# Performance work log

Hardware: AMD Instinct MI355X
Metric: run time of the kernel (lower is better)

The kernel has to match this reference:

```python
import jax, jax.numpy as jnp
import numpy as np

H, W, D = 60, 60, 36            # voxel grid dims (x, y, z)
GRID = 0.08                      # voxel size in meters
SCALE_MULT = 3.0                 # radius multiplier
CHUNK = 7200                     # point-chunk size; 129600 / 7200 = 18 chunks
P = 2048                         # number of Gaussians
C = 13                           # semantic channels


def setup_inputs() -> dict:
    key = jax.random.key(0)
    k1, k2, k3, k4, k5 = jax.random.split(key, 5)
    # query points = voxel centers, guaranteed in-range for the int-bin asserts
    ii, jj, kk = jnp.meshgrid(jnp.arange(H), jnp.arange(W), jnp.arange(D), indexing='ij')
    pts = (jnp.stack([ii, jj, kk], axis=-1).reshape(-1, 3).astype(jnp.float32) + 0.5) * GRID
    pts = pts[None]  # [1, N, 3]
    lo = jnp.array([0.1, 0.1, 0.1], jnp.float32)
    hi = jnp.array([H, W, D], jnp.float32) * GRID - 0.1
    means3D = jax.random.uniform(k1, (1, P, 3), dtype=jnp.float32) * (hi - lo) + lo
    scales = jax.random.uniform(k2, (1, P, 3), minval=0.03, maxval=0.2, dtype=jnp.float32)
    # random rotations via QR -> SPD covariance Sigma = Q diag(s^2) Q^T
    A = jax.random.normal(k3, (P, 3, 3), dtype=jnp.float32)
    Q, _ = jnp.linalg.qr(A)
    cov3D = jnp.einsum('pij,pj,pkj->pik', Q, scales[0] ** 2, Q)[None]  # [1,P,3,3]
    opacities = jax.random.uniform(k4, (1, P), minval=0.1, maxval=1.0, dtype=jnp.float32)
    semantics = jax.random.normal(k5, (1, P, C), dtype=jnp.float32)
    origin_use = jnp.zeros((3,), jnp.float32)
    return {"pts": pts, "means3D": means3D, "opacities": opacities,
            "semantics": semantics, "scales": scales, "cov3D": cov3D,
            "origin_use": origin_use}


def _sym_inv6(packed):
    # packed: [P,6] = (xx, yy, zz, xy, yz, xz) of a symmetric 3x3 covariance
    a, b, c, d, e, f = (packed[:, i] for i in range(6))
    det = a * (b * c - e * e) - d * (d * c - e * f) + f * (d * e - b * f)
    ixx = (b * c - e * e) / det
    iyy = (a * c - f * f) / det
    izz = (a * b - d * d) / det
    ixy = (e * f - d * c) / det
    iyz = (d * f - a * e) / det
    ixz = (d * e - b * f) / det
    return ixx, iyy, izz, ixy, iyz, ixz


def _forward(pts, means3D, opacities, semantics, scales, cov3D, origin_use):
    pts = pts[0]                    # [N,3], no grad in original
    means3D = means3D[0]            # [P,3]
    opacities = opacities[0]        # [P]
    semantics = semantics[0]        # [P,C]
    scales = jax.lax.stop_gradient(scales[0])   # detached in original
    cov3D = cov3D[0]                # [P,3,3]

    radii = jnp.ceil(scales.max(-1) * SCALE_MULT / GRID).astype(jnp.int32)  # [P]
    m_int = ((jax.lax.stop_gradient(means3D) - origin_use) / GRID).astype(jnp.int32)  # [P,3]
    packed = cov3D.reshape(-1, 9)[:, jnp.array([0, 4, 8, 1, 5, 2])]  # [P,6]
    ixx, iyy, izz, ixy, iyz, ixz = _sym_inv6(packed)  # per-Gaussian inverse cov entries

    N = pts.shape[0]
    pts_c = pts.reshape(N // CHUNK, CHUNK, 3)

    def chunk_fn(p):  # p: [CHUNK,3]
        p_int = ((p - origin_use) / GRID).astype(jnp.int32)
        dx = p[:, 0:1] - means3D[None, :, 0]   # [CHUNK,P]
        dy = p[:, 1:2] - means3D[None, :, 1]
        dz = p[:, 2:3] - means3D[None, :, 2]
        quad = (ixx * dx * dx + iyy * dy * dy + izz * dz * dz
                + 2.0 * (ixy * dx * dy + iyz * dy * dz + ixz * dx * dz))
        inbox = (jnp.abs(p_int[:, None, :] - m_int[None, :, :])
                 <= radii[None, :, None]).all(-1)          # [CHUNK,P] box/bin test
        w = jnp.where(inbox, opacities[None, :] * jnp.exp(-0.5 * quad), 0.0)
        return w @ semantics                                # [CHUNK,C]

    logits = jax.lax.map(chunk_fn, pts_c).reshape(N, C)
    return logits


def reference(pts, means3D, opacities, semantics, scales, cov3D, origin_use):
    return _forward(pts, means3D, opacities, semantics, scales, cov3D, origin_use)
```

## Files before the change

### kernel.cpp

```cpp
#include <hip/hip_runtime.h>


constexpr int   HH      = 60;
constexpr int   WW      = 60;
constexpr int   DD      = 36;
constexpr int   P_N     = 2048;
constexpr int   C_N     = 13;
constexpr int   BXD     = 15;
constexpr int   BYD     = 15;
constexpr int   BZD     = 9;
constexpr int   NBRICK  = BXD * BYD * BZD;
constexpr int   CAP     = 192;
constexpr float GRID_SZ = 0.08f;

__global__ __launch_bounds__(256) void agg_fused(const float* __restrict__ means,
                                                 const float* __restrict__ opac,
                                                 const float* __restrict__ sem,
                                                 const float* __restrict__ scales,
                                                 const float* __restrict__ cov,
                                                 const float* __restrict__ origin,
                                                 float* __restrict__ out) {
    __shared__ int    s_idx[CAP];
    __shared__ int    s_cnt;
    __shared__ float4 s_mem[CAP * 6];
    float (*s_acc)[64][C_N] = (float (*)[64][C_N])s_mem;

    const int b = (int)blockIdx.x;
    const int bk = b % BZD; const int rem = b / BZD;
    const int bj = rem % BYD; const int bi = rem / BYD;
    const int i0 = bi * 4, j0 = bj * 4, k0 = bk * 4;

    const float ox = origin[0], oy = origin[1], oz = origin[2];

    if (threadIdx.x == 0) s_cnt = 0;
    __syncthreads();

    for (int g = (int)threadIdx.x; g < P_N; g += 256) {
        const float mx = means[g * 3 + 0], my = means[g * 3 + 1], mz = means[g * 3 + 2];
        const float sx = scales[g * 3 + 0], sy = scales[g * 3 + 1], sz = scales[g * 3 + 2];
        const float smax = fmaxf(sx, fmaxf(sy, sz));
        const int rad = (int)ceilf(smax * 3.0f / GRID_SZ);
        const int mix = (int)((mx - ox) / GRID_SZ);
        const int miy = (int)((my - oy) / GRID_SZ);
        const int miz = (int)((mz - oz) / GRID_SZ);
        const bool ov = (mix - rad <= i0 + 3) && (mix + rad >= i0)
                     && (miy - rad <= j0 + 3) && (miy + rad >= j0)
                     && (miz - rad <= k0 + 3) && (miz + rad >= k0);
        if (ov) {
            int xlo = max(mix - rad - i0, 0), xhi = min(mix + rad - i0, 3);
            int ylo = max(miy - rad - j0, 0), yhi = min(miy + rad - j0, 3);
            int zlo = max(miz - rad - k0, 0), zhi = min(miz + rad - k0, 3);
            unsigned mx4 = (0xFu >> (3 - xhi)) & (0xFu << xlo);
            unsigned my4 = (0xFu >> (3 - yhi)) & (0xFu << ylo);
            unsigned mz4 = (0xFu >> (3 - zhi)) & (0xFu << zlo);
            unsigned ent = (unsigned)g | (mx4 << 12) | (my4 << 16) | (mz4 << 20);
            int t = atomicAdd(&s_cnt, 1);
            if (t < CAP) s_idx[t] = (int)ent;
        }
    }
    __syncthreads();
    const int cnt = min(s_cnt, CAP);

    for (int e = (int)threadIdx.x; e < cnt; e += 256) {
        const int ent = s_idx[e];
        const int g = ent & 0xFFF;
        const float* cv = cov + g * 9;
        const float a = cv[0], bb = cv[4], c = cv[8], d = cv[1], e5 = cv[5], f = cv[2];
        const float det = a * (bb * c - e5 * e5) - d * (d * c - e5 * f)
                        + f * (d * e5 - bb * f);
        const float kD = -0.5f * 1.44269504088896340736f;
        const float kO = -1.44269504088896340736f;
        float4 r0, r1, r2, r3, r4, r5;
        r0.x = means[g * 3 + 0]; r0.y = means[g * 3 + 1]; r0.z = means[g * 3 + 2];
        r0.w = __log2f(opac[g]);
        r1.x = kD * (bb * c - e5 * e5) / det;
        r1.y = kD * (a * c - f * f) / det;
        r1.z = kD * (a * bb - d * d) / det;
        r1.w = kO * (e5 * f - d * c) / det;
        r2.x = kO * (d * f - a * e5) / det;
        r2.y = kO * (d * e5 - bb * f) / det;
        const float* sm = sem + g * C_N;
        r2.z = sm[0];  r2.w = sm[1];
        r3.x = sm[2];  r3.y = sm[3];  r3.z = sm[4];  r3.w = sm[5];
        r4.x = sm[6];  r4.y = sm[7];  r4.z = sm[8];  r4.w = sm[9];
        r5.x = sm[10]; r5.y = sm[11]; r5.z = sm[12];
        r5.w = __int_as_float(ent);
        float4* dst = &s_mem[e * 6];
        dst[0] = r0; dst[1] = r1; dst[2] = r2; dst[3] = r3; dst[4] = r4; dst[5] = r5;
    }
    __syncthreads();

    const int wave = (int)threadIdx.x >> 6;
    const int lane = (int)threadIdx.x & 63;
    const int kk = lane & 3, lj = (lane >> 2) & 3, li = lane >> 4;
    const int gi = i0 + li, gj = j0 + lj, k = k0 + kk;
    const float px = ((float)gi + 0.5f) * GRID_SZ;
    const float py = ((float)gj + 0.5f) * GRID_SZ;
    const float pz = ((float)k  + 0.5f) * GRID_SZ;
    const unsigned sel = (1u << (12 + li)) | (1u << (16 + lj)) | (1u << (20 + kk));

    float acc[C_N];
#pragma unroll
    for (int cc = 0; cc < C_N; ++cc) acc[cc] = 0.0f;

#pragma unroll 2
    for (int i = wave; i < cnt; i += 4) {
        const float4 r0 = s_mem[i * 6 + 0];
        const float4 r1 = s_mem[i * 6 + 1];
        const float4 r2 = s_mem[i * 6 + 2];
        const float4 r3 = s_mem[i * 6 + 3];
        const float4 r4 = s_mem[i * 6 + 4];
        const float4 r5 = s_mem[i * 6 + 5];
        const unsigned ent = (unsigned)__float_as_int(r5.w);
        const bool inbox = (ent & sel) == sel;
        const float dx = px - r0.x, dy = py - r0.y, dz = pz - r0.z;
        float e2 = r0.w;
        e2 = fmaf(r1.x, dx * dx, e2);
        e2 = fmaf(r1.y, dy * dy, e2);
        e2 = fmaf(r1.z, dz * dz, e2);
        e2 = fmaf(r1.w, dx * dy, e2);
        e2 = fmaf(r2.x, dy * dz, e2);
        e2 = fmaf(r2.y, dx * dz, e2);
        float w = __builtin_amdgcn_exp2f(e2);
        w = inbox ? w : 0.0f;
        acc[0]  = fmaf(w, r2.z, acc[0]);
        acc[1]  = fmaf(w, r2.w, acc[1]);
        acc[2]  = fmaf(w, r3.x, acc[2]);
        acc[3]  = fmaf(w, r3.y, acc[3]);
        acc[4]  = fmaf(w, r3.z, acc[4]);
        acc[5]  = fmaf(w, r3.w, acc[5]);
        acc[6]  = fmaf(w, r4.x, acc[6]);
        acc[7]  = fmaf(w, r4.y, acc[7]);
        acc[8]  = fmaf(w, r4.z, acc[8]);
        acc[9]  = fmaf(w, r4.w, acc[9]);
        acc[10] = fmaf(w, r5.x, acc[10]);
        acc[11] = fmaf(w, r5.y, acc[11]);
        acc[12] = fmaf(w, r5.z, acc[12]);
    }

    __syncthreads();
#pragma unroll
    for (int cc = 0; cc < C_N; ++cc) (*(&s_acc[wave]))[lane][cc] = acc[cc];
    __syncthreads();

    for (int t = (int)threadIdx.x; t < 64 * C_N; t += 256) {
        const int v = t / C_N, c = t % C_N;
        const float s = s_acc[0][v][c] + s_acc[1][v][c]
                      + s_acc[2][v][c] + s_acc[3][v][c];
        const int vk = v & 3, vj = (v >> 2) & 3, vi = v >> 4;
        const long n = (long)(i0 + vi) * (WW * DD)
                     + (long)(j0 + vj) * DD + (k0 + vk);
        out[n * C_N + c] = s;
    }
}

extern "C" void kernel_launch(void* const* d_in, const int* in_sizes, int n_in,
                              void* d_out, int out_size, void* d_ws, size_t ws_size,
                              hipStream_t stream) {
    const float* means  = (const float*)d_in[1];
    const float* opac   = (const float*)d_in[2];
    const float* sem    = (const float*)d_in[3];
    const float* scales = (const float*)d_in[4];
    const float* cov    = (const float*)d_in[5];
    const float* origin = (const float*)d_in[6];
    float* out = (float*)d_out;

    agg_fused<<<NBRICK, 256, 0, stream>>>(means, opac, sem, scales, cov,
                                          origin, out);
}
```

Measured before the change: 87.93 us.

## Enlarge bricks along z and register-block three voxels per thread

```diff
diff --git a/kernel.cpp b/kernel.cpp
--- a/kernel.cpp
+++ b/kernel.cpp
@@ -8,9 +8,10 @@
 constexpr int   C_N     = 13;
 constexpr int   BXD     = 15;
 constexpr int   BYD     = 15;
-constexpr int   BZD     = 9;
+constexpr int   BZD     = 3;
+constexpr int   ZCH     = 12;
 constexpr int   NBRICK  = BXD * BYD * BZD;
-constexpr int   CAP     = 192;
+constexpr int   CAP     = 256;
 constexpr float GRID_SZ = 0.08f;
 
 __global__ __launch_bounds__(256) void agg_fused(const float* __restrict__ means,
@@ -26,9 +27,11 @@
     float (*s_acc)[64][C_N] = (float (*)[64][C_N])s_mem;
 
     const int b = (int)blockIdx.x;
-    const int bk = b % BZD; const int rem = b / BZD;
-    const int bj = rem % BYD; const int bi = rem / BYD;
-    const int i0 = bi * 4, j0 = bj * 4, k0 = bk * 4;
+    const int bz = b % BZD;
+    const int txy = b / BZD;
+    const int bj = txy % BYD;
+    const int bi = txy / BYD;
+    const int i0 = bi * 4, j0 = bj * 4, k0 = bz * ZCH;
 
     const float ox = origin[0], oy = origin[1], oz = origin[2];
 
@@ -43,17 +46,17 @@
         const int mix = (int)((mx - ox) / GRID_SZ);
         const int miy = (int)((my - oy) / GRID_SZ);
         const int miz = (int)((mz - oz) / GRID_SZ);
-        const bool ov = (mix - rad <= i0 + 3) && (mix + rad >= i0)
-                     && (miy - rad <= j0 + 3) && (miy + rad >= j0)
-                     && (miz - rad <= k0 + 3) && (miz + rad >= k0);
+        const bool ov = (mix - rad <= i0 + 3)       && (mix + rad >= i0)
+                     && (miy - rad <= j0 + 3)       && (miy + rad >= j0)
+                     && (miz - rad <= k0 + ZCH - 1) && (miz + rad >= k0);
         if (ov) {
             int xlo = max(mix - rad - i0, 0), xhi = min(mix + rad - i0, 3);
             int ylo = max(miy - rad - j0, 0), yhi = min(miy + rad - j0, 3);
-            int zlo = max(miz - rad - k0, 0), zhi = min(miz + rad - k0, 3);
-            unsigned mx4 = (0xFu >> (3 - xhi)) & (0xFu << xlo);
-            unsigned my4 = (0xFu >> (3 - yhi)) & (0xFu << ylo);
-            unsigned mz4 = (0xFu >> (3 - zhi)) & (0xFu << zlo);
-            unsigned ent = (unsigned)g | (mx4 << 12) | (my4 << 16) | (mz4 << 20);
+            int zlo = max(miz - rad - k0, 0), zhi = min(miz + rad - k0, ZCH - 1);
+            unsigned mx4  = (0xFu >> (3 - xhi)) & (0xFu << xlo);
+            unsigned my4  = (0xFu >> (3 - yhi)) & (0xFu << ylo);
+            unsigned mz12 = (0xFFFu >> (ZCH - 1 - zhi)) & (0xFFFu << zlo);
+            unsigned ent = (unsigned)g | (mx4 << 11) | (my4 << 15) | (mz12 << 19);
             int t = atomicAdd(&s_cnt, 1);
             if (t < CAP) s_idx[t] = (int)ent;
         }
@@ -63,7 +66,7 @@
 
     for (int e = (int)threadIdx.x; e < cnt; e += 256) {
         const int ent = s_idx[e];
-        const int g = ent & 0xFFF;
+        const int g = ent & 0x7FF;
         const float* cv = cov + g * 9;
         const float a = cv[0], bb = cv[4], c = cv[8], d = cv[1], e5 = cv[5], f = cv[2];
         const float det = a * (bb * c - e5 * e5) - d * (d * c - e5 * f)
@@ -93,15 +96,22 @@
     const int wave = (int)threadIdx.x >> 6;
     const int lane = (int)threadIdx.x & 63;
     const int kk = lane & 3, lj = (lane >> 2) & 3, li = lane >> 4;
-    const int gi = i0 + li, gj = j0 + lj, k = k0 + kk;
+    const int gi = i0 + li, gj = j0 + lj;
     const float px = ((float)gi + 0.5f) * GRID_SZ;
     const float py = ((float)gj + 0.5f) * GRID_SZ;
-    const float pz = ((float)k  + 0.5f) * GRID_SZ;
-    const unsigned sel = (1u << (12 + li)) | (1u << (16 + lj)) | (1u << (20 + kk));
+    float    pzv[3];
+    unsigned selv[3];
+#pragma unroll
+    for (int p = 0; p < 3; ++p) {
+        pzv[p]  = ((float)(k0 + kk + 4 * p) + 0.5f) * GRID_SZ;
+        selv[p] = (1u << (11 + li)) | (1u << (15 + lj)) | (1u << (19 + kk + 4 * p));
+    }
 
-    float acc[C_N];
+    float acc[3][C_N];
 #pragma unroll
-    for (int cc = 0; cc < C_N; ++cc) acc[cc] = 0.0f;
+    for (int p = 0; p < 3; ++p)
+#pragma unroll
+        for (int cc = 0; cc < C_N; ++cc) acc[p][cc] = 0.0f;
 
 #pragma unroll 2
     for (int i = wave; i < cnt; i += 4) {
@@ -112,45 +122,55 @@
         const float4 r4 = s_mem[i * 6 + 4];
         const float4 r5 = s_mem[i * 6 + 5];
         const unsigned ent = (unsigned)__float_as_int(r5.w);
-        const bool inbox = (ent & sel) == sel;
-        const float dx = px - r0.x, dy = py - r0.y, dz = pz - r0.z;
-        float e2 = r0.w;
-        e2 = fmaf(r1.x, dx * dx, e2);
-        e2 = fmaf(r1.y, dy * dy, e2);
-        e2 = fmaf(r1.z, dz * dz, e2);
-        e2 = fmaf(r1.w, dx * dy, e2);
-        e2 = fmaf(r2.x, dy * dz, e2);
-        e2 = fmaf(r2.y, dx * dz, e2);
-        float w = __builtin_amdgcn_exp2f(e2);
-        w = inbox ? w : 0.0f;
-        acc[0]  = fmaf(w, r2.z, acc[0]);
-        acc[1]  = fmaf(w, r2.w, acc[1]);
-        acc[2]  = fmaf(w, r3.x, acc[2]);
-        acc[3]  = fmaf(w, r3.y, acc[3]);
-        acc[4]  = fmaf(w, r3.z, acc[4]);
-        acc[5]  = fmaf(w, r3.w, acc[5]);
-        acc[6]  = fmaf(w, r4.x, acc[6]);
-        acc[7]  = fmaf(w, r4.y, acc[7]);
-        acc[8]  = fmaf(w, r4.z, acc[8]);
-        acc[9]  = fmaf(w, r4.w, acc[9]);
-        acc[10] = fmaf(w, r5.x, acc[10]);
-        acc[11] = fmaf(w, r5.y, acc[11]);
-        acc[12] = fmaf(w, r5.z, acc[12]);
+        const float dx = px - r0.x, dy = py - r0.y;
+        float base2 = r0.w;
+        base2 = fmaf(r1.x, dx * dx, base2);
+        base2 = fmaf(r1.y, dy * dy, base2);
+        base2 = fmaf(r1.w, dx * dy, base2);
+        float w[3];
+#pragma unroll
+        for (int p = 0; p < 3; ++p) {
+            const float dz = pzv[p] - r0.z;
+            float e2 = base2;
+            e2 = fmaf(r1.z, dz * dz, e2);
+            e2 = fmaf(r2.x, dy * dz, e2);
+            e2 = fmaf(r2.y, dx * dz, e2);
+            const float ww = __builtin_amdgcn_exp2f(e2);
+            w[p] = ((ent & selv[p]) == selv[p]) ? ww : 0.0f;
+        }
+#pragma unroll
+        for (int p = 0; p < 3; ++p) {
+            acc[p][0]  = fmaf(w[p], r2.z, acc[p][0]);
+            acc[p][1]  = fmaf(w[p], r2.w, acc[p][1]);
+            acc[p][2]  = fmaf(w[p], r3.x, acc[p][2]);
+            acc[p][3]  = fmaf(w[p], r3.y, acc[p][3]);
+            acc[p][4]  = fmaf(w[p], r3.z, acc[p][4]);
+            acc[p][5]  = fmaf(w[p], r3.w, acc[p][5]);
+            acc[p][6]  = fmaf(w[p], r4.x, acc[p][6]);
+            acc[p][7]  = fmaf(w[p], r4.y, acc[p][7]);
+            acc[p][8]  = fmaf(w[p], r4.z, acc[p][8]);
+            acc[p][9]  = fmaf(w[p], r4.w, acc[p][9]);
+            acc[p][10] = fmaf(w[p], r5.x, acc[p][10]);
+            acc[p][11] = fmaf(w[p], r5.y, acc[p][11]);
+            acc[p][12] = fmaf(w[p], r5.z, acc[p][12]);
+        }
     }
 
-    __syncthreads();
 #pragma unroll
-    for (int cc = 0; cc < C_N; ++cc) (*(&s_acc[wave]))[lane][cc] = acc[cc];
-    __syncthreads();
-
-    for (int t = (int)threadIdx.x; t < 64 * C_N; t += 256) {
-        const int v = t / C_N, c = t % C_N;
-        const float s = s_acc[0][v][c] + s_acc[1][v][c]
-                      + s_acc[2][v][c] + s_acc[3][v][c];
-        const int vk = v & 3, vj = (v >> 2) & 3, vi = v >> 4;
-        const long n = (long)(i0 + vi) * (WW * DD)
-                     + (long)(j0 + vj) * DD + (k0 + vk);
-        out[n * C_N + c] = s;
+    for (int p = 0; p < 3; ++p) {
+        __syncthreads();
+#pragma unroll
+        for (int cc = 0; cc < C_N; ++cc) s_acc[wave][lane][cc] = acc[p][cc];
+        __syncthreads();
+        for (int t = (int)threadIdx.x; t < 64 * C_N; t += 256) {
+            const int v = t / C_N, c = t % C_N;
+            const float s = s_acc[0][v][c] + s_acc[1][v][c]
+                          + s_acc[2][v][c] + s_acc[3][v][c];
+            const int vk = v & 3, vj = (v >> 2) & 3, vi = v >> 4;
+            const long n = (long)(i0 + vi) * (WW * DD)
+                         + (long)(j0 + vj) * DD + (k0 + vk + 4 * p);
+            out[n * C_N + c] = s;
+        }
     }
 }
 
```

New measurement: 87.21 us. Within noise of the previous version (-0.8%).
